# Performance work log

Measured on AMD Instinct MI355X. Metric: run time of the kernel, lower is better.

The kernel has to match this reference:

```python
import jax, jax.numpy as jnp
import numpy as np

HEAD_DIM = 64
EMBED_DIM = 1024

def setup_inputs() -> dict:
    key = jax.random.key(0)
    k1, k2, k3, k4 = jax.random.split(key, 4)
    x = jax.random.normal(k1, (4, 4096, EMBED_DIM), dtype=jnp.float32)
    # nn.Linear(embed_dim, head_dim, bias=False): weight shape (head_dim, embed_dim)
    s = 1.0 / np.sqrt(EMBED_DIM)
    Wq = jax.random.uniform(k2, (HEAD_DIM, EMBED_DIM), jnp.float32, -s, s)
    Wk = jax.random.uniform(k3, (HEAD_DIM, EMBED_DIM), jnp.float32, -s, s)
    Wv = jax.random.uniform(k4, (HEAD_DIM, EMBED_DIM), jnp.float32, -s, s)
    return {"x": x, "Wq": Wq, "Wk": Wk, "Wv": Wv}

def reference(x, Wq, Wk, Wv):
    # Faithful to source: V = self.key(x), i.e. uses Wk (Wv is an unused param).
    n_ctx = x.shape[1]
    Q = jnp.einsum('bse,de->bsd', x, Wq)
    K = jnp.einsum('bse,de->bsd', x, Wk)
    V = jnp.einsum('bse,de->bsd', x, Wk)
    scale = 1.0 / jnp.sqrt(jnp.asarray(K.shape[-1], x.dtype))
    scores = jnp.einsum('bqd,bkd->bqk', Q, K) * scale  # [b, n_ctx, n_ctx]
    causal = jnp.tril(jnp.ones((n_ctx, n_ctx), dtype=bool))
    scores = jnp.where(causal, scores, jnp.asarray(-jnp.inf, scores.dtype))
    attn = jax.nn.softmax(scores, axis=-1)
    # dropout(p=0.2) omitted: reference runs in eval mode (identity)
    out = jnp.einsum('bqk,bkd->bqd', attn, V)
    return out
```

## Files before the change

kernel.cpp:

```cpp
#include <hip/hip_runtime.h>

typedef _Float16 f16;
typedef _Float16 f16x8 __attribute__((ext_vector_type(8)));
typedef _Float16 f16x4 __attribute__((ext_vector_type(4)));
typedef float f32x4 __attribute__((ext_vector_type(4)));

#define S_LEN 4096
#define B_SZ  4
#define E_DIM 1024
#define D_DIM 64
#define NROWS (B_SZ * S_LEN)
#define NSPLIT 4
#define QSCALE (0.125f * 1.44269504088896f)
#define SMAX 8.0f

__device__ __forceinline__ float exp2g(float x) { return __builtin_amdgcn_exp2f(x); }

__global__ __launch_bounds__(256) void wpack_kernel(const float* __restrict__ Wq,
                                                    const float* __restrict__ Wk,
                                                    f16* __restrict__ Bp) {
    int id = blockIdx.x * 256 + threadIdx.x;
    int lane = id & 63, kc = (id >> 6) & 31, n = id >> 11;
    int row = n * 16 + (lane & 15);
    int col = kc * 32 + (lane >> 4) * 8;
    const float* src = (row < 64) ? (Wq + (long)row * E_DIM + col)
                                  : (Wk + (long)(row - 64) * E_DIM + col);
    float4 v0 = ((const float4*)src)[0];
    float4 v1 = ((const float4*)src)[1];
    f16x8 h = {(f16)v0.x, (f16)v0.y, (f16)v0.z, (f16)v0.w,
               (f16)v1.x, (f16)v1.y, (f16)v1.z, (f16)v1.w};
    *(f16x8*)(Bp + (long)id * 8) = h;
}

__global__ __launch_bounds__(256, 4) void proj_kernel(const float* __restrict__ x,
                                                      const f16* __restrict__ Bp,
                                                      f16* __restrict__ Qh,
                                                      f16* __restrict__ Kh) {
    __shared__ union {
        f16   xs[16][1040];
        float rb[4][16][132];
    } sm;

    const int tid  = threadIdx.x;
    const int w    = tid >> 6;
    const int lane = tid & 63;
    const int l15  = lane & 15;
    const int quad = lane >> 4;
    const long m0  = (long)blockIdx.x * 16;

#pragma unroll
    for (int c = 0; c < 16; c++) {
        int f4 = c * 256 + tid;
        int row = f4 >> 8;
        int col = (f4 & 255) * 4;
        float4 v = *(const float4*)(x + (m0 + row) * E_DIM + col);
        f16x4 h = {(f16)v.x, (f16)v.y, (f16)v.z, (f16)v.w};
        *(f16x4*)&sm.xs[row][col] = h;
    }
    __syncthreads();

    f32x4 acc[8];
#pragma unroll
    for (int n = 0; n < 8; n++) acc[n] = (f32x4){0.f, 0.f, 0.f, 0.f};

    const int kc0 = w * 8;
#pragma unroll
    for (int s = 0; s < 8; s++) {
        f16x8 a = *(const f16x8*)&sm.xs[l15][w * 256 + s * 32 + quad * 8];
#pragma unroll
        for (int n = 0; n < 8; n++) {
            f16x8 b = *(const f16x8*)(Bp + (((long)n * 32 + kc0 + s) * 64 + lane) * 8);
            acc[n] = __builtin_amdgcn_mfma_f32_16x16x32_f16(a, b, acc[n], 0, 0, 0);
        }
    }
    __syncthreads();

#pragma unroll
    for (int n = 0; n < 8; n++)
#pragma unroll
        for (int r = 0; r < 4; r++)
            sm.rb[w][quad * 4 + r][n * 16 + l15] = acc[n][r];
    __syncthreads();

    const int row = tid >> 4;
    const int c0  = (tid & 15) * 8;
    float sum[8];
#pragma unroll
    for (int i = 0; i < 8; i++) sum[i] = 0.f;
#pragma unroll
    for (int w4 = 0; w4 < 4; w4++)
#pragma unroll
        for (int g = 0; g < 2; g++) {
            f32x4 u = *(const f32x4*)&sm.rb[w4][row][c0 + g * 4];
#pragma unroll
            for (int i = 0; i < 4; i++) sum[g * 4 + i] += u[i];
        }

    const long grow = m0 + row;
    f16 tmp[8];
    if (c0 < 64) {
#pragma unroll
        for (int i = 0; i < 8; i++) tmp[i] = (f16)(sum[i] * QSCALE);
        *(f16x8*)(Qh + grow * 64 + c0) = *(f16x8*)tmp;
    } else {
#pragma unroll
        for (int i = 0; i < 8; i++) tmp[i] = (f16)sum[i];
        *(f16x8*)(Kh + grow * 64 + (c0 - 64)) = *(f16x8*)tmp;
    }
}

__global__ __launch_bounds__(256, 4) void attn_kernel(const f16* __restrict__ Qh,
                                                      const f16* __restrict__ Kh,
                                                      float* __restrict__ OutP0,
                                                      f16* __restrict__ P123,
                                                      float* __restrict__ Ml) {
    __shared__ __align__(16) f16 Kr[64][72];
    __shared__ __align__(16) f16 Kt[64][72];
    __shared__ __align__(16) f16 Pm[64][88];

    const int tid  = threadIdx.x;
    const int w    = tid >> 6;
    const int lane = tid & 63;
    const int l15  = lane & 15;
    const int quad = lane >> 4;

    const int bid  = blockIdx.x;
    const int qraw = bid & 63;
    const int half = (bid >> 6) & 3;
    const int b    = bid >> 8;
    const int qt   = (b & 1) ? (63 - qraw) : qraw;
    const long q0  = (long)qt * 64;

    const f16* Qb = Qh + (long)b * S_LEN * 64;
    const f16* Kb = Kh + (long)b * S_LEN * 64;

    f16x8 Aq[2];
#pragma unroll
    for (int kf = 0; kf < 2; kf++)
        Aq[kf] = *(const f16x8*)(Qb + (q0 + w * 16 + l15) * 64 + kf * 32 + quad * 8);

    const f16x8 ones = {(f16)1.f, (f16)1.f, (f16)1.f, (f16)1.f,
                        (f16)1.f, (f16)1.f, (f16)1.f, (f16)1.f};

    f32x4 O[4];
    f32x4 Lacc = (f32x4){0.f, 0.f, 0.f, 0.f};
#pragma unroll
    for (int n = 0; n < 4; n++) O[n] = (f32x4){0.f, 0.f, 0.f, 0.f};

    f16x8 pre[2];
    if (half <= qt) {
#pragma unroll
        for (int it = 0; it < 2; it++)
            pre[it] = *(const f16x8*)(Kb + ((long)half * 64 + lane) * 64 + (w + it * 4) * 8);
    }

    for (int j = half; j <= qt; j += NSPLIT) {
        __syncthreads();
#pragma unroll
        for (int it = 0; it < 2; it++) {
            int sg = w + it * 4;
            *(f16x8*)&Kr[lane][sg * 8] = pre[it];
#pragma unroll
            for (int i = 0; i < 8; i++) Kt[sg * 8 + i][lane] = pre[it][i];
        }
        if (j + NSPLIT <= qt) {
#pragma unroll
            for (int it = 0; it < 2; it++)
                pre[it] = *(const f16x8*)(Kb + ((long)(j + NSPLIT) * 64 + lane) * 64 + (w + it * 4) * 8);
        }
        __syncthreads();

        f32x4 S[4];
#pragma unroll
        for (int n = 0; n < 4; n++) S[n] = (f32x4){0.f, 0.f, 0.f, 0.f};
#pragma unroll
        for (int n = 0; n < 4; n++)
#pragma unroll
            for (int kf = 0; kf < 2; kf++) {
                f16x8 bfr = *(const f16x8*)&Kr[n * 16 + l15][kf * 32 + quad * 8];
                S[n] = __builtin_amdgcn_mfma_f32_16x16x32_f16(Aq[kf], bfr, S[n], 0, 0, 0);
            }

        if (j == qt) {
#pragma unroll
            for (int n = 0; n < 4; n++) {
                int col_rel = n * 16 + l15;
#pragma unroll
                for (int r = 0; r < 4; r++)
                    if (col_rel > w * 16 + quad * 4 + r) S[n][r] = -1e30f;
            }
        }

#pragma unroll
        for (int n = 0; n < 4; n++)
#pragma unroll
            for (int r = 0; r < 4; r++)
                Pm[w * 16 + quad * 4 + r][n * 16 + l15] = (f16)exp2g(S[n][r] - SMAX);

#pragma unroll
        for (int kf = 0; kf < 2; kf++) {
            f16x8 pa = *(const f16x8*)&Pm[w * 16 + l15][kf * 32 + quad * 8];
            Lacc = __builtin_amdgcn_mfma_f32_16x16x32_f16(pa, ones, Lacc, 0, 0, 0);
#pragma unroll
            for (int n = 0; n < 4; n++) {
                f16x8 vb = *(const f16x8*)&Kt[n * 16 + l15][kf * 32 + quad * 8];
                O[n] = __builtin_amdgcn_mfma_f32_16x16x32_f16(pa, vb, O[n], 0, 0, 0);
            }
        }
    }

    const long growbase = (long)b * S_LEN + q0;
#pragma unroll
    for (int r = 0; r < 4; r++) {
        long grow = growbase + w * 16 + quad * 4 + r;
        if (half == 0) {
#pragma unroll
            for (int n = 0; n < 4; n++) OutP0[grow * 64 + n * 16 + l15] = O[n][r];
        } else {
            f16* dst = P123 + (long)(half - 1) * NROWS * 64;
#pragma unroll
            for (int n = 0; n < 4; n++) dst[grow * 64 + n * 16 + l15] = (f16)O[n][r];
        }
        if (l15 == 0) Ml[(long)half * NROWS + grow] = Lacc[r];
    }
}

__global__ __launch_bounds__(256) void combine_kernel(float* __restrict__ Out,
                                                      const f16* __restrict__ P123,
                                                      const float* __restrict__ Ml) {
    int gid = blockIdx.x * 256 + threadIdx.x;
    long row = gid >> 4;
    int c0 = (gid & 15) * 4;
    float lt = 0.f;
#pragma unroll
    for (int h = 0; h < 4; h++) lt += Ml[(long)h * NROWS + row];
    float inv = 1.0f / lt;

    float* p = Out + row * 64 + c0;
    float4 res = *(const float4*)p;
#pragma unroll
    for (int h = 1; h < 4; h++) {
        f16x4 oh = *(const f16x4*)(P123 + (long)(h - 1) * NROWS * 64 + row * 64 + c0);
        res.x += (float)oh[0];
        res.y += (float)oh[1];
        res.z += (float)oh[2];
        res.w += (float)oh[3];
    }
    *(float4*)p = make_float4(res.x * inv, res.y * inv, res.z * inv, res.w * inv);
}

extern "C" void kernel_launch(void* const* d_in, const int* in_sizes, int n_in,
                              void* d_out, int out_size, void* d_ws, size_t ws_size,
                              hipStream_t stream) {
    const float* x  = (const float*)d_in[0];
    const float* Wq = (const float*)d_in[1];
    const float* Wk = (const float*)d_in[2];
    float* out = (float*)d_out;

    f16* Qh    = (f16*)d_ws;
    f16* Kh    = Qh + (long)NROWS * D_DIM;
    f16* Bp    = Kh + (long)NROWS * D_DIM;
    f16* P123  = Bp + (long)128 * E_DIM;
    float* Ml  = (float*)(P123 + 3L * NROWS * D_DIM);

    wpack_kernel<<<dim3(64), dim3(256), 0, stream>>>(Wq, Wk, Bp);
    proj_kernel<<<dim3(NROWS / 16), dim3(256), 0, stream>>>(x, Bp, Qh, Kh);
    attn_kernel<<<dim3(64 * NSPLIT * B_SZ), dim3(256), 0, stream>>>(Qh, Kh, out, P123, Ml);
    combine_kernel<<<dim3(NROWS * 16 / 256), dim3(256), 0, stream>>>(out, P123, Ml);
}
```

Before: 133.6 us.

## Enlarge projection and attention tiles, split N across waves, double-buffer K tiles

The projection kernel now handles 32 rows per block and splits output columns across waves, so each wave accumulates over the full K dimension. This removes the cross-wave LDS reduction. The attention kernel processes 128 query rows per block, so each K tile loaded into LDS is reused by twice as many rows. It double-buffers the K tiles to drop one barrier per iteration, orders blocks so the longest causal rows are scheduled first, skips fully masked diagonal sub-tiles per wave, and raises MFMA priority with s_setprio. In exchange it uses more registers and LDS, which lowers occupancy (launch bounds go from 4 to 2), and launches fewer blocks.

```diff
diff --git a/kernel.cpp b/kernel.cpp
--- a/kernel.cpp
+++ b/kernel.cpp
@@ -32,13 +32,13 @@
     *(f16x8*)(Bp + (long)id * 8) = h;
 }
 
-__global__ __launch_bounds__(256, 4) void proj_kernel(const float* __restrict__ x,
+__global__ __launch_bounds__(256, 2) void proj_kernel(const float* __restrict__ x,
                                                       const f16* __restrict__ Bp,
                                                       f16* __restrict__ Qh,
                                                       f16* __restrict__ Kh) {
     __shared__ union {
-        f16   xs[16][1040];
-        float rb[4][16][132];
+        f16 xs[32][1032];
+        f16 os[32][136];
     } sm;
 
     const int tid  = threadIdx.x;
@@ -46,77 +46,75 @@
     const int lane = tid & 63;
     const int l15  = lane & 15;
     const int quad = lane >> 4;
-    const long m0  = (long)blockIdx.x * 16;
+    const long m0  = (long)blockIdx.x * 32;
 
 #pragma unroll
     for (int c = 0; c < 16; c++) {
-        int f4 = c * 256 + tid;
-        int row = f4 >> 8;
-        int col = (f4 & 255) * 4;
-        float4 v = *(const float4*)(x + (m0 + row) * E_DIM + col);
-        f16x4 h = {(f16)v.x, (f16)v.y, (f16)v.z, (f16)v.w};
-        *(f16x4*)&sm.xs[row][col] = h;
+        int f8 = c * 256 + tid;
+        int row = f8 >> 7;
+        int col = (f8 & 127) * 8;
+        const float* src = x + (m0 + row) * E_DIM + col;
+        float4 v0 = ((const float4*)src)[0];
+        float4 v1 = ((const float4*)src)[1];
+        f16x8 h = {(f16)v0.x, (f16)v0.y, (f16)v0.z, (f16)v0.w,
+                   (f16)v1.x, (f16)v1.y, (f16)v1.z, (f16)v1.w};
+        *(f16x8*)&sm.xs[row][col] = h;
     }
     __syncthreads();
 
-    f32x4 acc[8];
-#pragma unroll
-    for (int n = 0; n < 8; n++) acc[n] = (f32x4){0.f, 0.f, 0.f, 0.f};
-
-    const int kc0 = w * 8;
-#pragma unroll
-    for (int s = 0; s < 8; s++) {
-        f16x8 a = *(const f16x8*)&sm.xs[l15][w * 256 + s * 32 + quad * 8];
-#pragma unroll
-        for (int n = 0; n < 8; n++) {
-            f16x8 b = *(const f16x8*)(Bp + (((long)n * 32 + kc0 + s) * 64 + lane) * 8);
-            acc[n] = __builtin_amdgcn_mfma_f32_16x16x32_f16(a, b, acc[n], 0, 0, 0);
+    f32x4 acc[2][2];
+#pragma unroll
+    for (int m = 0; m < 2; m++)
+#pragma unroll
+        for (int nn = 0; nn < 2; nn++) acc[m][nn] = (f32x4){0.f, 0.f, 0.f, 0.f};
+
+    const int n0 = w * 2;
+#pragma unroll 4
+    for (int kc = 0; kc < 32; kc++) {
+        f16x8 a0 = *(const f16x8*)&sm.xs[l15][kc * 32 + quad * 8];
+        f16x8 a1 = *(const f16x8*)&sm.xs[16 + l15][kc * 32 + quad * 8];
+#pragma unroll
+        for (int nn = 0; nn < 2; nn++) {
+            f16x8 b = *(const f16x8*)(Bp + (((long)(n0 + nn) * 32 + kc) * 64 + lane) * 8);
+            acc[0][nn] = __builtin_amdgcn_mfma_f32_16x16x32_f16(a0, b, acc[0][nn], 0, 0, 0);
+            acc[1][nn] = __builtin_amdgcn_mfma_f32_16x16x32_f16(a1, b, acc[1][nn], 0, 0, 0);
         }
     }
     __syncthreads();
 
 #pragma unroll
-    for (int n = 0; n < 8; n++)
-#pragma unroll
-        for (int r = 0; r < 4; r++)
-            sm.rb[w][quad * 4 + r][n * 16 + l15] = acc[n][r];
+    for (int m = 0; m < 2; m++)
+#pragma unroll
+        for (int nn = 0; nn < 2; nn++) {
+            int colg = w * 32 + nn * 16 + l15;
+            float sc = (colg < 64) ? QSCALE : 1.0f;
+#pragma unroll
+            for (int r = 0; r < 4; r++)
+                sm.os[m * 16 + quad * 4 + r][colg] = (f16)(acc[m][nn][r] * sc);
+        }
     __syncthreads();
 
-    const int row = tid >> 4;
-    const int c0  = (tid & 15) * 8;
-    float sum[8];
-#pragma unroll
-    for (int i = 0; i < 8; i++) sum[i] = 0.f;
-#pragma unroll
-    for (int w4 = 0; w4 < 4; w4++)
-#pragma unroll
-        for (int g = 0; g < 2; g++) {
-            f32x4 u = *(const f32x4*)&sm.rb[w4][row][c0 + g * 4];
-#pragma unroll
-            for (int i = 0; i < 4; i++) sum[g * 4 + i] += u[i];
-        }
-
-    const long grow = m0 + row;
-    f16 tmp[8];
-    if (c0 < 64) {
-#pragma unroll
-        for (int i = 0; i < 8; i++) tmp[i] = (f16)(sum[i] * QSCALE);
-        *(f16x8*)(Qh + grow * 64 + c0) = *(f16x8*)tmp;
-    } else {
-#pragma unroll
-        for (int i = 0; i < 8; i++) tmp[i] = (f16)sum[i];
-        *(f16x8*)(Kh + grow * 64 + (c0 - 64)) = *(f16x8*)tmp;
-    }
-}
-
-__global__ __launch_bounds__(256, 4) void attn_kernel(const f16* __restrict__ Qh,
+    {
+        int row = tid >> 3, cg = tid & 7;
+        long grow = m0 + row;
+#pragma unroll
+        for (int h = 0; h < 2; h++) {
+            int col = cg * 16 + h * 8;
+            f16x8 v = *(const f16x8*)&sm.os[row][col];
+            if (col < 64) *(f16x8*)(Qh + grow * 64 + col)        = v;
+            else          *(f16x8*)(Kh + grow * 64 + (col - 64)) = v;
+        }
+    }
+}
+
+__global__ __launch_bounds__(256, 2) void attn_kernel(const f16* __restrict__ Qh,
                                                       const f16* __restrict__ Kh,
                                                       float* __restrict__ OutP0,
                                                       f16* __restrict__ P123,
                                                       float* __restrict__ Ml) {
-    __shared__ __align__(16) f16 Kr[64][72];
-    __shared__ __align__(16) f16 Kt[64][72];
-    __shared__ __align__(16) f16 Pm[64][88];
+    __shared__ __align__(16) f16 Kr[2][64][72];
+    __shared__ __align__(16) f16 Kt[2][64][72];
+    __shared__ __align__(16) f16 Pm[128][88];
 
     const int tid  = threadIdx.x;
     const int w    = tid >> 6;
@@ -125,104 +123,136 @@
     const int quad = lane >> 4;
 
     const int bid  = blockIdx.x;
-    const int qraw = bid & 63;
-    const int half = (bid >> 6) & 3;
-    const int b    = bid >> 8;
-    const int qt   = (b & 1) ? (63 - qraw) : qraw;
-    const long q0  = (long)qt * 64;
+    const int b    = bid & 3;
+    const int half = (bid >> 2) & 3;
+    const int qraw = bid >> 4;
+    const int qt   = 31 - qraw;
+    const long q0  = (long)qt * 128;
+    const int jmax = 2 * qt + 1;
 
     const f16* Qb = Qh + (long)b * S_LEN * 64;
     const f16* Kb = Kh + (long)b * S_LEN * 64;
 
-    f16x8 Aq[2];
-#pragma unroll
-    for (int kf = 0; kf < 2; kf++)
-        Aq[kf] = *(const f16x8*)(Qb + (q0 + w * 16 + l15) * 64 + kf * 32 + quad * 8);
+    f16x8 Aq[2][2];
+#pragma unroll
+    for (int m = 0; m < 2; m++)
+#pragma unroll
+        for (int kf = 0; kf < 2; kf++)
+            Aq[m][kf] = *(const f16x8*)(Qb + (q0 + w * 32 + m * 16 + l15) * 64 + kf * 32 + quad * 8);
 
     const f16x8 ones = {(f16)1.f, (f16)1.f, (f16)1.f, (f16)1.f,
                         (f16)1.f, (f16)1.f, (f16)1.f, (f16)1.f};
 
-    f32x4 O[4];
-    f32x4 Lacc = (f32x4){0.f, 0.f, 0.f, 0.f};
-#pragma unroll
-    for (int n = 0; n < 4; n++) O[n] = (f32x4){0.f, 0.f, 0.f, 0.f};
+    f32x4 O[2][4];
+    f32x4 Lacc[2];
+#pragma unroll
+    for (int m = 0; m < 2; m++) {
+        Lacc[m] = (f32x4){0.f, 0.f, 0.f, 0.f};
+#pragma unroll
+        for (int n = 0; n < 4; n++) O[m][n] = (f32x4){0.f, 0.f, 0.f, 0.f};
+    }
 
     f16x8 pre[2];
-    if (half <= qt) {
+    if (half <= jmax) {
 #pragma unroll
         for (int it = 0; it < 2; it++)
             pre[it] = *(const f16x8*)(Kb + ((long)half * 64 + lane) * 64 + (w + it * 4) * 8);
     }
 
-    for (int j = half; j <= qt; j += NSPLIT) {
-        __syncthreads();
+    int buf = 0;
+    for (int j = half; j <= jmax; j += NSPLIT) {
 #pragma unroll
         for (int it = 0; it < 2; it++) {
             int sg = w + it * 4;
-            *(f16x8*)&Kr[lane][sg * 8] = pre[it];
-#pragma unroll
-            for (int i = 0; i < 8; i++) Kt[sg * 8 + i][lane] = pre[it][i];
-        }
-        if (j + NSPLIT <= qt) {
+            *(f16x8*)&Kr[buf][lane][sg * 8] = pre[it];
+#pragma unroll
+            for (int i = 0; i < 8; i++) Kt[buf][sg * 8 + i][lane] = pre[it][i];
+        }
+        if (j + NSPLIT <= jmax) {
 #pragma unroll
             for (int it = 0; it < 2; it++)
                 pre[it] = *(const f16x8*)(Kb + ((long)(j + NSPLIT) * 64 + lane) * 64 + (w + it * 4) * 8);
         }
         __syncthreads();
 
-        f32x4 S[4];
-#pragma unroll
-        for (int n = 0; n < 4; n++) S[n] = (f32x4){0.f, 0.f, 0.f, 0.f};
-#pragma unroll
-        for (int n = 0; n < 4; n++)
+        const int odiag = j * 64 - (int)q0;
+        const bool alive = !(odiag == 64 && w < 2);
+        if (alive) {
+            f32x4 S[2][4];
+#pragma unroll
+            for (int m = 0; m < 2; m++)
+#pragma unroll
+                for (int n = 0; n < 4; n++) S[m][n] = (f32x4){0.f, 0.f, 0.f, 0.f};
+
+            __builtin_amdgcn_s_setprio(1);
+#pragma unroll
+            for (int n = 0; n < 4; n++)
+#pragma unroll
+                for (int kf = 0; kf < 2; kf++) {
+                    f16x8 bfr = *(const f16x8*)&Kr[buf][n * 16 + l15][kf * 32 + quad * 8];
+                    S[0][n] = __builtin_amdgcn_mfma_f32_16x16x32_f16(Aq[0][kf], bfr, S[0][n], 0, 0, 0);
+                    S[1][n] = __builtin_amdgcn_mfma_f32_16x16x32_f16(Aq[1][kf], bfr, S[1][n], 0, 0, 0);
+                }
+            __builtin_amdgcn_s_setprio(0);
+
+            if (odiag >= 0) {
+#pragma unroll
+                for (int m = 0; m < 2; m++) {
+                    int rbase = w * 32 + m * 16 + quad * 4;
+#pragma unroll
+                    for (int n = 0; n < 4; n++) {
+                        int colrel = odiag + n * 16 + l15;
+#pragma unroll
+                        for (int r = 0; r < 4; r++)
+                            if (colrel > rbase + r) S[m][n][r] = -1e30f;
+                    }
+                }
+            }
+
+#pragma unroll
+            for (int m = 0; m < 2; m++)
+#pragma unroll
+                for (int n = 0; n < 4; n++)
+#pragma unroll
+                    for (int r = 0; r < 4; r++)
+                        Pm[w * 32 + m * 16 + quad * 4 + r][n * 16 + l15] =
+                            (f16)exp2g(S[m][n][r] - SMAX);
+
+            __builtin_amdgcn_s_setprio(1);
 #pragma unroll
             for (int kf = 0; kf < 2; kf++) {
-                f16x8 bfr = *(const f16x8*)&Kr[n * 16 + l15][kf * 32 + quad * 8];
-                S[n] = __builtin_amdgcn_mfma_f32_16x16x32_f16(Aq[kf], bfr, S[n], 0, 0, 0);
+                f16x8 pa0 = *(const f16x8*)&Pm[w * 32 + l15][kf * 32 + quad * 8];
+                f16x8 pa1 = *(const f16x8*)&Pm[w * 32 + 16 + l15][kf * 32 + quad * 8];
+                Lacc[0] = __builtin_amdgcn_mfma_f32_16x16x32_f16(pa0, ones, Lacc[0], 0, 0, 0);
+                Lacc[1] = __builtin_amdgcn_mfma_f32_16x16x32_f16(pa1, ones, Lacc[1], 0, 0, 0);
+#pragma unroll
+                for (int n = 0; n < 4; n++) {
+                    f16x8 vb = *(const f16x8*)&Kt[buf][n * 16 + l15][kf * 32 + quad * 8];
+                    O[0][n] = __builtin_amdgcn_mfma_f32_16x16x32_f16(pa0, vb, O[0][n], 0, 0, 0);
+                    O[1][n] = __builtin_amdgcn_mfma_f32_16x16x32_f16(pa1, vb, O[1][n], 0, 0, 0);
+                }
             }
-
-        if (j == qt) {
-#pragma unroll
-            for (int n = 0; n < 4; n++) {
-                int col_rel = n * 16 + l15;
-#pragma unroll
-                for (int r = 0; r < 4; r++)
-                    if (col_rel > w * 16 + quad * 4 + r) S[n][r] = -1e30f;
+            __builtin_amdgcn_s_setprio(0);
+        }
+        buf ^= 1;
+    }
+
+    const long growbase = (long)b * S_LEN + q0;
+#pragma unroll
+    for (int m = 0; m < 2; m++)
+#pragma unroll
+        for (int r = 0; r < 4; r++) {
+            long grow = growbase + w * 32 + m * 16 + quad * 4 + r;
+            if (half == 0) {
+#pragma unroll
+                for (int n = 0; n < 4; n++) OutP0[grow * 64 + n * 16 + l15] = O[m][n][r];
+            } else {
+                f16* dst = P123 + (long)(half - 1) * NROWS * 64;
+#pragma unroll
+                for (int n = 0; n < 4; n++) dst[grow * 64 + n * 16 + l15] = (f16)O[m][n][r];
             }
-        }
-
-#pragma unroll
-        for (int n = 0; n < 4; n++)
-#pragma unroll
-            for (int r = 0; r < 4; r++)
-                Pm[w * 16 + quad * 4 + r][n * 16 + l15] = (f16)exp2g(S[n][r] - SMAX);
-
-#pragma unroll
-        for (int kf = 0; kf < 2; kf++) {
-            f16x8 pa = *(const f16x8*)&Pm[w * 16 + l15][kf * 32 + quad * 8];
-            Lacc = __builtin_amdgcn_mfma_f32_16x16x32_f16(pa, ones, Lacc, 0, 0, 0);
-#pragma unroll
-            for (int n = 0; n < 4; n++) {
-                f16x8 vb = *(const f16x8*)&Kt[n * 16 + l15][kf * 32 + quad * 8];
-                O[n] = __builtin_amdgcn_mfma_f32_16x16x32_f16(pa, vb, O[n], 0, 0, 0);
-            }
-        }
-    }
-
-    const long growbase = (long)b * S_LEN + q0;
-#pragma unroll
-    for (int r = 0; r < 4; r++) {
-        long grow = growbase + w * 16 + quad * 4 + r;
-        if (half == 0) {
-#pragma unroll
-            for (int n = 0; n < 4; n++) OutP0[grow * 64 + n * 16 + l15] = O[n][r];
-        } else {
-            f16* dst = P123 + (long)(half - 1) * NROWS * 64;
-#pragma unroll
-            for (int n = 0; n < 4; n++) dst[grow * 64 + n * 16 + l15] = (f16)O[n][r];
-        }
-        if (l15 == 0) Ml[(long)half * NROWS + grow] = Lacc[r];
-    }
+            if (l15 == 0) Ml[(long)half * NROWS + grow] = Lacc[m][r];
+        }
 }
 
 __global__ __launch_bounds__(256) void combine_kernel(float* __restrict__ Out,
@@ -264,7 +294,7 @@
     float* Ml  = (float*)(P123 + 3L * NROWS * D_DIM);
 
     wpack_kernel<<<dim3(64), dim3(256), 0, stream>>>(Wq, Wk, Bp);
-    proj_kernel<<<dim3(NROWS / 16), dim3(256), 0, stream>>>(x, Bp, Qh, Kh);
-    attn_kernel<<<dim3(64 * NSPLIT * B_SZ), dim3(256), 0, stream>>>(Qh, Kh, out, P123, Ml);
+    proj_kernel<<<dim3(NROWS / 32), dim3(256), 0, stream>>>(x, Bp, Qh, Kh);
+    attn_kernel<<<dim3(32 * NSPLIT * B_SZ), dim3(256), 0, stream>>>(Qh, Kh, out, P123, Ml);
     combine_kernel<<<dim3(NROWS * 16 / 256), dim3(256), 0, stream>>>(out, P123, Ml);
 }
```

New measurement: 131.6 us. No clear change (-1.5%).
